# Optimization experiments

Hardware: AMD Instinct MI355X
Metric: run time of the kernel (lower is better)

## Reference

```python
import jax, jax.numpy as jnp
import numpy as np

EPS = 1e-5

def _gcn_norm(edge_index, n):
    # Add self-loops, compute symmetric normalization deg^-1/2 * deg^-1/2 (PyG GCNConv).
    src = jnp.concatenate([edge_index[0], jnp.arange(n)])
    dst = jnp.concatenate([edge_index[1], jnp.arange(n)])
    deg = jax.ops.segment_sum(jnp.ones_like(dst, dtype=jnp.float32), dst, num_segments=n)
    dinv = jnp.where(deg > 0, jax.lax.rsqrt(deg), 0.0)
    norm = dinv[src] * dinv[dst]  # [E + N]
    return src, dst, norm

def _gcn_conv(x, W, b, src, dst, norm, n):
    h = x @ W                      # linear first (out_dim < in_dim here)
    msg = h[src] * norm[:, None]   # gather + per-edge scale
    out = jax.ops.segment_sum(msg, dst, num_segments=n)  # scatter-add aggregation
    return out + b

def _bn(x, g, b):
    # BatchNorm over nodes (training-mode batch statistics, biased variance)
    mu = x.mean(axis=0)
    var = jnp.mean((x - mu) ** 2, axis=0)
    return (x - mu) * jax.lax.rsqrt(var + EPS) * g + b


def setup_inputs() -> dict:
    key = jax.random.key(0)
    N, E, F_in = 10000, 320000, 256
    ks = jax.random.split(key, 8)
    dims = [F_in, 220, 150, 100, 60, 17]
    inp = {
        'x': jax.random.normal(ks[0], (N, F_in), dtype=jnp.float32),
        'edge_index': jax.random.randint(ks[1], (2, E), 0, N, dtype=jnp.int64),
    }
    for i in range(5):
        fan_in, fan_out = dims[i], dims[i + 1]
        scale = 1.0 / np.sqrt(fan_in)
        inp[f'W{i+1}'] = jax.random.normal(ks[2 + i], (fan_in, fan_out), dtype=jnp.float32) * scale
        inp[f'b{i+1}'] = jnp.zeros((fan_out,), dtype=jnp.float32)
    for i, d in enumerate([220, 150, 100, 60]):
        inp[f'g{i+1}'] = jnp.ones((d,), dtype=jnp.float32)
        inp[f'be{i+1}'] = jnp.zeros((d,), dtype=jnp.float32)
    return inp


def reference(x, edge_index, W1, b1, W2, b2, W3, b3, W4, b4, W5, b5,
              g1, be1, g2, be2, g3, be3, g4, be4):
    n = x.shape[0]
    src, dst, norm = _gcn_norm(edge_index, n)
    h = _gcn_conv(x, W1, b1, src, dst, norm, n)
    h = _bn(jax.nn.relu(h), g1, be1)
    # dropout omitted (eval-mode identity)
    h = _gcn_conv(h, W2, b2, src, dst, norm, n)
    h = _bn(jax.nn.relu(h), g2, be2)
    h = _gcn_conv(h, W3, b3, src, dst, norm, n)
    h = _bn(jax.nn.relu(h), g3, be3)
    h = _gcn_conv(h, W4, b4, src, dst, norm, n)
    h = _bn(jax.nn.relu(h), g4, be4)
    h = _gcn_conv(h, W5, b5, src, dst, norm, n)
    return jax.nn.log_softmax(h, axis=1)
```

## Files before the change

kernel.cpp:

```cpp
#include <hip/hip_runtime.h>
#include <math.h>

typedef unsigned short ushort_t;
typedef unsigned int uint_t;
typedef unsigned long long ull_t;

__device__ __forceinline__ float bf2f(ushort_t u) {
    union { uint_t i; float f; } x; x.i = ((uint_t)u) << 16; return x.f;
}
__device__ __forceinline__ ushort_t f2bf(float f) {
    union { float f; uint_t i; } x; x.f = f;
    uint_t r = x.i + 0x7FFFu + ((x.i >> 16) & 1u);
    return (ushort_t)(r >> 16);
}

__global__ __launch_bounds__(256) void k_init(
    int* __restrict__ cnt, float* __restrict__ stats, float* __restrict__ wbias, int N)
{
    const int gt = blockIdx.x * 256 + threadIdx.x;
    const int gth = gridDim.x * 256;
    for (int i = gt; i < N; i += gth) cnt[i] = 0;
    for (int i = gt; i < 2048; i += gth) stats[i] = 0.f;
    if (gt < 256) wbias[gt] = 0.f;
}

__global__ __launch_bounds__(256) void k_hist_prep0(
    const int* __restrict__ dst, int* __restrict__ cnt, int E, int eBlk,
    const float* __restrict__ W0, ushort_t* __restrict__ Wt)
{
    if ((int)blockIdx.x < eBlk) {
        int e = blockIdx.x * 256 + threadIdx.x;
        if (e < E) atomicAdd(&cnt[dst[e]], 1);
    } else {
        int base = ((int)blockIdx.x - eBlk) * 256 + (int)threadIdx.x;
        for (int idx = base; idx < 224 * 256; idx += 56 * 256) {
            int j = idx >> 8;
            int k = idx & 255;
            float v = (j < 220) ? W0[(long)k * 220 + j] : 0.f;
            Wt[idx] = f2bf(v);
        }
    }
}

__global__ __launch_bounds__(1024) void k_scan(
    const int* __restrict__ cnt, int* __restrict__ row_start,
    int* __restrict__ cursor, float* __restrict__ dinv, int N)
{
    __shared__ int sh[1024];
    const int tid = threadIdx.x;
    const int chunk = (N + 1023) >> 10;
    int loc[16];
    const int base = tid * chunk;
    int sum = 0;
    for (int c = 0; c < chunk; ++c) {
        int i = base + c;
        int v = (i < N) ? cnt[i] : 0;
        loc[c] = sum;
        sum += v;
    }
    sh[tid] = sum;
    __syncthreads();
    for (int off = 1; off < 1024; off <<= 1) {
        int v = (tid >= off) ? sh[tid - off] : 0;
        __syncthreads();
        sh[tid] += v;
        __syncthreads();
    }
    const int excl = sh[tid] - sum;
    for (int c = 0; c < chunk; ++c) {
        int i = base + c;
        if (i < N) {
            int rs = excl + loc[c];
            row_start[i] = rs;
            cursor[i] = rs;
            dinv[i] = rsqrtf(1.0f + (float)cnt[i]);
        }
    }
    if (tid == 1023) row_start[N] = sh[1023];
}

__global__ void k_prep(const float* __restrict__ W,
                       const float* __restrict__ g, const float* __restrict__ be,
                       const float* __restrict__ cs, const float* __restrict__ cq,
                       ushort_t* __restrict__ Wt, float* __restrict__ wbias,
                       int K, int M, int Kp, int Mp, int yW, float invN)
{
    __shared__ float sm[256];
    if ((int)blockIdx.y < yW) {
        if (threadIdx.y == 0) {
            int kk = blockIdx.x * 64 + threadIdx.x;
            float sc = 0.f;
            if (kk < K) {
                float mu = cs[kk] * invN;
                float var = cq[kk] * invN - mu * mu;
                sc = g[kk] * rsqrtf(var + 1e-5f);
            }
            sm[threadIdx.x] = sc;
        }
        __syncthreads();
        int k = blockIdx.x * 64 + threadIdx.x;
        int j = blockIdx.y * 4 + threadIdx.y;
        if (k >= Kp || j >= Mp) return;
        float v = 0.f;
        if (k < K && j < M) v = sm[threadIdx.x] * W[(long)k * M + j];
        Wt[(long)j * Kp + k] = f2bf(v);
    } else {
        __shared__ float red[4][64];
        int t = threadIdx.y * 64 + threadIdx.x;
        for (int kk = t; kk < K; kk += 256) {
            float mu = cs[kk] * invN;
            float var = cq[kk] * invN - mu * mu;
            float sc = g[kk] * rsqrtf(var + 1e-5f);
            sm[kk] = be[kk] - mu * sc;
        }
        __syncthreads();
        int jl = t & 63, kg = t >> 6;
        int j = blockIdx.x * 64 + jl;
        float s = 0.f;
        if (j < M) {
            for (int k = kg; k < K; k += 4) s += sm[k] * W[(long)k * M + j];
        }
        red[kg][jl] = s;
        __syncthreads();
        if (kg == 0 && j < Mp) wbias[j] = red[0][jl] + red[1][jl] + red[2][jl] + red[3][jl];
    }
}

template<int KP, bool F32A, bool FILL>
__global__ __launch_bounds__(256) void k_gemm_mfma(
    const void* __restrict__ Xin, const ushort_t* __restrict__ Wt,
    const float* __restrict__ wbias, const float* __restrict__ dinv,
    ushort_t* __restrict__ h2, int N, int Mp,
    int gx, const int* __restrict__ fsrc, const int* __restrict__ fdst,
    int* __restrict__ fcursor, int* __restrict__ fcsr, int fE)
{
    typedef __attribute__((ext_vector_type(8))) short short8;
    typedef __attribute__((ext_vector_type(4))) float floatx4;
    constexpr int LSTR = KP + 16;
    __shared__ ushort_t Bs[64 * LSTR];

    if (FILL) {
        if ((int)blockIdx.x >= gx) {
            const int fid = ((int)blockIdx.x - gx) * (int)gridDim.y + (int)blockIdx.y;
            const int e = fid * 256 + (int)threadIdx.x;
            if (e < fE) {
                int pos = atomicAdd(&fcursor[fdst[e]], 1);
                fcsr[pos] = fsrc[e];
            }
            return;
        }
    }

    const int tid = threadIdx.x;
    const int wave = tid >> 6, lane = tid & 63;
    const int m = lane & 15, quad = lane >> 4;
    const int i0 = blockIdx.x * 64 + wave * 16;
    const int j0 = blockIdx.y * 64;
    const int ncols = min(64, Mp - j0);
    const int ntiles = ncols >> 4;

    {
        const int cpr = KP / 8;
        const int chunks = ncols * cpr;
        for (int c = tid; c < chunks; c += 256) {
            int jj = c / cpr;
            int kk = (c - jj * cpr) * 8;
            *(short8*)(Bs + jj * LSTR + kk) =
                *(const short8*)(Wt + (long)(j0 + jj) * KP + kk);
        }
    }
    __syncthreads();

    if (i0 >= N) return;

    floatx4 acc[4];
    #pragma unroll
    for (int t = 0; t < 4; ++t) { acc[t].x = 0.f; acc[t].y = 0.f; acc[t].z = 0.f; acc[t].w = 0.f; }

    const int ra = min(i0 + m, N - 1);
    const ushort_t* arow_h = F32A ? nullptr : (const ushort_t*)Xin + (long)ra * KP + quad * 8;
    const float*    arow_f = F32A ? (const float*)Xin + (long)ra * KP + quad * 8 : nullptr;

    #pragma unroll
    for (int k0 = 0; k0 < KP; k0 += 32) {
        short8 av;
        if (F32A) {
            float4 f0 = *(const float4*)(arow_f + k0);
            float4 f1 = *(const float4*)(arow_f + k0 + 4);
            av[0] = (short)f2bf(f0.x); av[1] = (short)f2bf(f0.y);
            av[2] = (short)f2bf(f0.z); av[3] = (short)f2bf(f0.w);
            av[4] = (short)f2bf(f1.x); av[5] = (short)f2bf(f1.y);
            av[6] = (short)f2bf(f1.z); av[7] = (short)f2bf(f1.w);
        } else {
            av = *(const short8*)(arow_h + k0);
        }
        #pragma unroll
        for (int t = 0; t < 4; ++t) {
            if (t < ntiles) {
                short8 bv = *(const short8*)(Bs + (t * 16 + m) * LSTR + k0 + quad * 8);
                acc[t] = __builtin_amdgcn_mfma_f32_16x16x32_bf16(av, bv, acc[t], 0, 0, 0);
            }
        }
    }

    #pragma unroll
    for (int t = 0; t < 4; ++t) {
        if (t < ntiles) {
            int j = j0 + t * 16 + m;
            float wb = wbias[j];
            #pragma unroll
            for (int r = 0; r < 4; ++r) {
                int i = i0 + quad * 4 + r;
                if (i < N) h2[(long)i * Mp + j] = f2bf((acc[t][r] + wb) * dinv[i]);
            }
        }
    }
}

__global__ __launch_bounds__(256) void k_agg(
    const int* __restrict__ row_start, const int* __restrict__ csr_src,
    const ushort_t* __restrict__ h2, int hs,
    const float* __restrict__ dinv, const float* __restrict__ b,
    ushort_t* __restrict__ tmpb, int ts,
    float* __restrict__ cs, float* __restrict__ csq,
    int N, int M, int Q, ull_t magic, uint_t sh)
{
    __shared__ float s_s[256];
    __shared__ float s_q[256];
    const int tid = threadIdx.x;
    s_s[tid] = 0.f;
    s_q[tid] = 0.f;
    __syncthreads();

    const uint_t g = blockIdx.x * 256 + tid;
    const uint_t i = (uint_t)(((ull_t)g * magic) >> sh);
    const int jp = (int)(g - i * Q);
    const int j0 = jp * 8;
    float vals[8];
    bool active = false;

    if (i < (uint_t)N) {
        if (j0 >= M) {
            *(uint4*)(tmpb + (long)i * ts + j0) = make_uint4(0u, 0u, 0u, 0u);
        } else {
            active = true;
            const int s0 = row_start[i];
            const int s1 = row_start[i + 1];
            const ushort_t* hp = h2 + j0;
            float acc[8];
            {
                uint4 v = *(const uint4*)(hp + (long)i * hs);
                acc[0] = bf2f((ushort_t)(v.x & 0xffff)); acc[1] = bf2f((ushort_t)(v.x >> 16));
                acc[2] = bf2f((ushort_t)(v.y & 0xffff)); acc[3] = bf2f((ushort_t)(v.y >> 16));
                acc[4] = bf2f((ushort_t)(v.z & 0xffff)); acc[5] = bf2f((ushort_t)(v.z >> 16));
                acc[6] = bf2f((ushort_t)(v.w & 0xffff)); acc[7] = bf2f((ushort_t)(v.w >> 16));
            }
            int e = s0;
            for (; e + 3 < s1; e += 4) {
                int n0 = csr_src[e], n1 = csr_src[e + 1], n2 = csr_src[e + 2], n3 = csr_src[e + 3];
                uint4 w0 = *(const uint4*)(hp + (long)n0 * hs);
                uint4 w1 = *(const uint4*)(hp + (long)n1 * hs);
                uint4 w2 = *(const uint4*)(hp + (long)n2 * hs);
                uint4 w3 = *(const uint4*)(hp + (long)n3 * hs);
                acc[0] += bf2f((ushort_t)(w0.x & 0xffff)); acc[1] += bf2f((ushort_t)(w0.x >> 16));
                acc[2] += bf2f((ushort_t)(w0.y & 0xffff)); acc[3] += bf2f((ushort_t)(w0.y >> 16));
                acc[4] += bf2f((ushort_t)(w0.z & 0xffff)); acc[5] += bf2f((ushort_t)(w0.z >> 16));
                acc[6] += bf2f((ushort_t)(w0.w & 0xffff)); acc[7] += bf2f((ushort_t)(w0.w >> 16));
                acc[0] += bf2f((ushort_t)(w1.x & 0xffff)); acc[1] += bf2f((ushort_t)(w1.x >> 16));
                acc[2] += bf2f((ushort_t)(w1.y & 0xffff)); acc[3] += bf2f((ushort_t)(w1.y >> 16));
                acc[4] += bf2f((ushort_t)(w1.z & 0xffff)); acc[5] += bf2f((ushort_t)(w1.z >> 16));
                acc[6] += bf2f((ushort_t)(w1.w & 0xffff)); acc[7] += bf2f((ushort_t)(w1.w >> 16));
                acc[0] += bf2f((ushort_t)(w2.x & 0xffff)); acc[1] += bf2f((ushort_t)(w2.x >> 16));
                acc[2] += bf2f((ushort_t)(w2.y & 0xffff)); acc[3] += bf2f((ushort_t)(w2.y >> 16));
                acc[4] += bf2f((ushort_t)(w2.z & 0xffff)); acc[5] += bf2f((ushort_t)(w2.z >> 16));
                acc[6] += bf2f((ushort_t)(w2.w & 0xffff)); acc[7] += bf2f((ushort_t)(w2.w >> 16));
                acc[0] += bf2f((ushort_t)(w3.x & 0xffff)); acc[1] += bf2f((ushort_t)(w3.x >> 16));
                acc[2] += bf2f((ushort_t)(w3.y & 0xffff)); acc[3] += bf2f((ushort_t)(w3.y >> 16));
                acc[4] += bf2f((ushort_t)(w3.z & 0xffff)); acc[5] += bf2f((ushort_t)(w3.z >> 16));
                acc[6] += bf2f((ushort_t)(w3.w & 0xffff)); acc[7] += bf2f((ushort_t)(w3.w >> 16));
            }
            for (; e < s1; ++e) {
                uint4 w = *(const uint4*)(hp + (long)csr_src[e] * hs);
                acc[0] += bf2f((ushort_t)(w.x & 0xffff)); acc[1] += bf2f((ushort_t)(w.x >> 16));
                acc[2] += bf2f((ushort_t)(w.y & 0xffff)); acc[3] += bf2f((ushort_t)(w.y >> 16));
                acc[4] += bf2f((ushort_t)(w.z & 0xffff)); acc[5] += bf2f((ushort_t)(w.z >> 16));
                acc[6] += bf2f((ushort_t)(w.w & 0xffff)); acc[7] += bf2f((ushort_t)(w.w >> 16));
            }
            const float di = dinv[i];
            ushort_t r[8];
            #pragma unroll
            for (int u = 0; u < 8; ++u) {
                float v = (j0 + u < M) ? fmaxf(acc[u] * di + b[j0 + u], 0.f) : 0.f;
                vals[u] = v;
                r[u] = f2bf(v);
            }
            uint4 pk;
            pk.x = (uint_t)r[0] | ((uint_t)r[1] << 16);
            pk.y = (uint_t)r[2] | ((uint_t)r[3] << 16);
            pk.z = (uint_t)r[4] | ((uint_t)r[5] << 16);
            pk.w = (uint_t)r[6] | ((uint_t)r[7] << 16);
            *(uint4*)(tmpb + (long)i * ts + j0) = pk;
        }
    }

    if (active) {
        #pragma unroll
        for (int u = 0; u < 8; ++u) {
            atomicAdd(&s_s[j0 + u], vals[u]);
            atomicAdd(&s_q[j0 + u], vals[u] * vals[u]);
        }
    }
    __syncthreads();
    if (tid < ts && (s_s[tid] != 0.f || s_q[tid] != 0.f)) {
        unsafeAtomicAdd(&cs[tid], s_s[tid]);
        unsafeAtomicAdd(&csq[tid], s_q[tid]);
    }
}

__global__ __launch_bounds__(256) void k_agg_final(
    const int* __restrict__ row_start, const int* __restrict__ csr_src,
    const ushort_t* __restrict__ h2, const float* __restrict__ dinv,
    const float* __restrict__ b, float* __restrict__ out, int N, int M)
{
    const int x = threadIdx.x;
    const int i = blockIdx.x * 16 + threadIdx.y;
    if (i >= N) return;
    const int j0 = 2 * x, j1 = 2 * x + 1;
    uint_t v = *(const uint_t*)(h2 + (long)i * 32 + j0);
    float a0 = bf2f((ushort_t)(v & 0xffff));
    float a1 = bf2f((ushort_t)(v >> 16));
    const int s0 = row_start[i];
    const int s1 = row_start[i + 1];
    int e = s0;
    for (; e + 1 < s1; e += 2) {
        int n0 = csr_src[e], n1 = csr_src[e + 1];
        uint_t w0 = *(const uint_t*)(h2 + (long)n0 * 32 + j0);
        uint_t w1 = *(const uint_t*)(h2 + (long)n1 * 32 + j0);
        a0 += bf2f((ushort_t)(w0 & 0xffff)); a1 += bf2f((ushort_t)(w0 >> 16));
        a0 += bf2f((ushort_t)(w1 & 0xffff)); a1 += bf2f((ushort_t)(w1 >> 16));
    }
    for (; e < s1; ++e) {
        uint_t w = *(const uint_t*)(h2 + (long)csr_src[e] * 32 + j0);
        a0 += bf2f((ushort_t)(w & 0xffff)); a1 += bf2f((ushort_t)(w >> 16));
    }
    const float di = dinv[i];
    float r0 = (j0 < M) ? (a0 * di + b[j0]) : -INFINITY;
    float r1 = (j1 < M) ? (a1 * di + b[j1]) : -INFINITY;
    float m = fmaxf(r0, r1);
    #pragma unroll
    for (int msk = 1; msk < 16; msk <<= 1) m = fmaxf(m, __shfl_xor(m, msk, 16));
    float s = ((j0 < M) ? expf(r0 - m) : 0.f) + ((j1 < M) ? expf(r1 - m) : 0.f);
    #pragma unroll
    for (int msk = 1; msk < 16; msk <<= 1) s += __shfl_xor(s, msk, 16);
    const float l = logf(s) + m;
    if (j0 < M) out[(long)i * M + j0] = r0 - l;
    if (j1 < M) out[(long)i * M + j1] = r1 - l;
}


static inline int pad16(int v) { return (v + 15) & ~15; }
static inline int pad32(int v) { return (v + 31) & ~31; }

extern "C" void kernel_launch(void* const* d_in, const int* in_sizes, int n_in,
                              void* d_out, int out_size, void* d_ws, size_t ws_size,
                              hipStream_t stream)
{
    const int dims[6] = {256, 220, 150, 100, 60, 17};
    const int N = in_sizes[0] / dims[0];
    const int E = in_sizes[1] / 2;

    const float* x  = (const float*)d_in[0];
    const int* ei   = (const int*)d_in[1];
    const int* srcv = ei;
    const int* dstv = ei + E;
    const float* Wl[5], *bl[5];
    for (int l = 0; l < 5; ++l) {
        Wl[l] = (const float*)d_in[2 + 2 * l];
        bl[l] = (const float*)d_in[3 + 2 * l];
    }
    const float* gl[4], *bel[4];
    for (int l = 0; l < 4; ++l) {
        gl[l]  = (const float*)d_in[12 + 2 * l];
        bel[l] = (const float*)d_in[13 + 2 * l];
    }
    float* out = (float*)d_out;

    char* w = (char*)d_ws;
    const long NB  = ((long)N * 4 + 255) & ~255L;
    const long NB1 = ((long)(N + 1) * 4 + 255) & ~255L;
    const long EB  = ((long)E * 4 + 255) & ~255L;
    const long FBB = ((long)N * 224 * 2 + 255) & ~255L;
    const long WTB = ((long)224 * 256 * 2 + 255) & ~255L;

    long o = 0;
    float* dinv      = (float*)(w + o);  o += NB;
    float* stats     = (float*)(w + o);  o += 2048 * 4;
    float* wbias     = (float*)(w + o);  o += 1024;
    int*   cnt       = (int*)(w + o);    o += NB;
    int*   row_start = (int*)(w + o);    o += NB1;
    int*   cursor    = (int*)(w + o);    o += NB;
    int*   csr_src   = (int*)(w + o);    o += EB;
    ushort_t* Wt     = (ushort_t*)(w + o); o += WTB;
    ushort_t* h2     = (ushort_t*)(w + o); o += FBB;
    ushort_t* tmpb   = (ushort_t*)(w + o); o += FBB;

    const int eBlk = (E + 255) / 256;
    const float invN = 1.0f / (float)N;

    k_init<<<(N + 255) / 256, 256, 0, stream>>>(cnt, stats, wbias, N);
    k_hist_prep0<<<eBlk + 56, 256, 0, stream>>>(dstv, cnt, E, eBlk, Wl[0], Wt);
    k_scan<<<1, 1024, 0, stream>>>(cnt, row_start, cursor, dinv, N);

    for (int l = 0; l < 5; ++l) {
        const int K  = dims[l];
        const int M  = dims[l + 1];
        const int Kp = pad32(K);
        const int Mp = pad16(M);
        const int ts = (l < 4) ? pad32(M) : 32;

        if (l > 0) {
            const int yW = (Mp + 3) / 4;
            k_prep<<<dim3((Kp + 63) / 64, yW + 1), dim3(64, 4), 0, stream>>>(
                Wl[l], gl[l - 1], bel[l - 1],
                stats + (l - 1) * 512, stats + (l - 1) * 512 + 256,
                Wt, wbias, K, M, Kp, Mp, yW, invN);
        }

        dim3 gg((N + 63) / 64, (Mp + 63) / 64);
        if (l == 0) {
            const int fx = (eBlk + (int)gg.y - 1) / (int)gg.y;
            dim3 gg0(gg.x + fx, gg.y);
            k_gemm_mfma<256, true, true><<<gg0, 256, 0, stream>>>(
                x, Wt, wbias, dinv, h2, N, Mp,
                (int)gg.x, srcv, dstv, cursor, csr_src, E);
        } else {
            switch (Kp) {
                case 224: k_gemm_mfma<224, false, false><<<gg, 256, 0, stream>>>(
                    tmpb, Wt, wbias, dinv, h2, N, Mp, 0, nullptr, nullptr, nullptr, nullptr, 0); break;
                case 160: k_gemm_mfma<160, false, false><<<gg, 256, 0, stream>>>(
                    tmpb, Wt, wbias, dinv, h2, N, Mp, 0, nullptr, nullptr, nullptr, nullptr, 0); break;
                case 128: k_gemm_mfma<128, false, false><<<gg, 256, 0, stream>>>(
                    tmpb, Wt, wbias, dinv, h2, N, Mp, 0, nullptr, nullptr, nullptr, nullptr, 0); break;
                case  64: k_gemm_mfma< 64, false, false><<<gg, 256, 0, stream>>>(
                    tmpb, Wt, wbias, dinv, h2, N, Mp, 0, nullptr, nullptr, nullptr, nullptr, 0); break;
            }
        }

        if (l < 4) {
            const int Q = ts / 8;
            uint_t shmt = 0;
            while ((1u << shmt) < (uint_t)Q) ++shmt;
            shmt += 32;
            const ull_t magic = ((1ULL << shmt) + Q - 1) / (ull_t)Q;
            const long total = (long)N * Q;
            k_agg<<<(int)((total + 255) / 256), 256, 0, stream>>>(
                row_start, csr_src, h2, Mp, dinv, bl[l], tmpb, ts,
                stats + l * 512, stats + l * 512 + 256,
                N, M, Q, magic, shmt);
        } else {
            k_agg_final<<<(N + 15) / 16, dim3(16, 16), 0, stream>>>(
                row_start, csr_src, h2, dinv, bl[l], out, N, M);
        }
    }
}
```

Measured before the change: 384.3 us.

## Split neighbor aggregation across four lanes per output chunk with shuffle reduction

```diff
diff --git a/kernel.cpp b/kernel.cpp
--- a/kernel.cpp
+++ b/kernel.cpp
@@ -223,7 +223,7 @@
     const float* __restrict__ dinv, const float* __restrict__ b,
     ushort_t* __restrict__ tmpb, int ts,
     float* __restrict__ cs, float* __restrict__ csq,
-    int N, int M, int Q, ull_t magic, uint_t sh)
+    int N, int M, int P, ull_t magic, uint_t sh)
 {
     __shared__ float s_s[256];
     __shared__ float s_q[256];
@@ -234,30 +234,35 @@
 
     const uint_t g = blockIdx.x * 256 + tid;
     const uint_t i = (uint_t)(((ull_t)g * magic) >> sh);
-    const int jp = (int)(g - i * Q);
+    const int r = (int)(g - i * (uint_t)P);
+    const int jp = r >> 2;
+    const int half = r & 3;
     const int j0 = jp * 8;
     float vals[8];
     bool active = false;
 
     if (i < (uint_t)N) {
         if (j0 >= M) {
-            *(uint4*)(tmpb + (long)i * ts + j0) = make_uint4(0u, 0u, 0u, 0u);
+            if (half == 0)
+                *(uint4*)(tmpb + (long)i * ts + j0) = make_uint4(0u, 0u, 0u, 0u);
         } else {
-            active = true;
             const int s0 = row_start[i];
             const int s1 = row_start[i + 1];
             const ushort_t* hp = h2 + j0;
             float acc[8];
-            {
+            if (half == 0) {
                 uint4 v = *(const uint4*)(hp + (long)i * hs);
                 acc[0] = bf2f((ushort_t)(v.x & 0xffff)); acc[1] = bf2f((ushort_t)(v.x >> 16));
                 acc[2] = bf2f((ushort_t)(v.y & 0xffff)); acc[3] = bf2f((ushort_t)(v.y >> 16));
                 acc[4] = bf2f((ushort_t)(v.z & 0xffff)); acc[5] = bf2f((ushort_t)(v.z >> 16));
                 acc[6] = bf2f((ushort_t)(v.w & 0xffff)); acc[7] = bf2f((ushort_t)(v.w >> 16));
-            }
-            int e = s0;
-            for (; e + 3 < s1; e += 4) {
-                int n0 = csr_src[e], n1 = csr_src[e + 1], n2 = csr_src[e + 2], n3 = csr_src[e + 3];
+            } else {
+                #pragma unroll
+                for (int u = 0; u < 8; ++u) acc[u] = 0.f;
+            }
+            int e = s0 + half;
+            for (; e + 12 < s1; e += 16) {
+                int n0 = csr_src[e], n1 = csr_src[e + 4], n2 = csr_src[e + 8], n3 = csr_src[e + 12];
                 uint4 w0 = *(const uint4*)(hp + (long)n0 * hs);
                 uint4 w1 = *(const uint4*)(hp + (long)n1 * hs);
                 uint4 w2 = *(const uint4*)(hp + (long)n2 * hs);
@@ -279,27 +284,35 @@
                 acc[4] += bf2f((ushort_t)(w3.z & 0xffff)); acc[5] += bf2f((ushort_t)(w3.z >> 16));
                 acc[6] += bf2f((ushort_t)(w3.w & 0xffff)); acc[7] += bf2f((ushort_t)(w3.w >> 16));
             }
-            for (; e < s1; ++e) {
+            for (; e < s1; e += 4) {
                 uint4 w = *(const uint4*)(hp + (long)csr_src[e] * hs);
                 acc[0] += bf2f((ushort_t)(w.x & 0xffff)); acc[1] += bf2f((ushort_t)(w.x >> 16));
                 acc[2] += bf2f((ushort_t)(w.y & 0xffff)); acc[3] += bf2f((ushort_t)(w.y >> 16));
                 acc[4] += bf2f((ushort_t)(w.z & 0xffff)); acc[5] += bf2f((ushort_t)(w.z >> 16));
                 acc[6] += bf2f((ushort_t)(w.w & 0xffff)); acc[7] += bf2f((ushort_t)(w.w >> 16));
             }
-            const float di = dinv[i];
-            ushort_t r[8];
             #pragma unroll
-            for (int u = 0; u < 8; ++u) {
-                float v = (j0 + u < M) ? fmaxf(acc[u] * di + b[j0 + u], 0.f) : 0.f;
-                vals[u] = v;
-                r[u] = f2bf(v);
-            }
-            uint4 pk;
-            pk.x = (uint_t)r[0] | ((uint_t)r[1] << 16);
-            pk.y = (uint_t)r[2] | ((uint_t)r[3] << 16);
-            pk.z = (uint_t)r[4] | ((uint_t)r[5] << 16);
-            pk.w = (uint_t)r[6] | ((uint_t)r[7] << 16);
-            *(uint4*)(tmpb + (long)i * ts + j0) = pk;
+            for (int u = 0; u < 8; ++u) acc[u] += __shfl_xor(acc[u], 1, 64);
+            #pragma unroll
+            for (int u = 0; u < 8; ++u) acc[u] += __shfl_xor(acc[u], 2, 64);
+
+            if (half == 0) {
+                const float di = dinv[i];
+                ushort_t rr[8];
+                #pragma unroll
+                for (int u = 0; u < 8; ++u) {
+                    float v = (j0 + u < M) ? fmaxf(acc[u] * di + b[j0 + u], 0.f) : 0.f;
+                    vals[u] = v;
+                    rr[u] = f2bf(v);
+                }
+                uint4 pk;
+                pk.x = (uint_t)rr[0] | ((uint_t)rr[1] << 16);
+                pk.y = (uint_t)rr[2] | ((uint_t)rr[3] << 16);
+                pk.z = (uint_t)rr[4] | ((uint_t)rr[5] << 16);
+                pk.w = (uint_t)rr[6] | ((uint_t)rr[7] << 16);
+                *(uint4*)(tmpb + (long)i * ts + j0) = pk;
+                active = true;
+            }
         }
     }
 
@@ -322,27 +335,37 @@
     const ushort_t* __restrict__ h2, const float* __restrict__ dinv,
     const float* __restrict__ b, float* __restrict__ out, int N, int M)
 {
-    const int x = threadIdx.x;
-    const int i = blockIdx.x * 16 + threadIdx.y;
+    const int tid = threadIdx.x;
+    const int lane = tid & 63;
+    const int wv = tid >> 6;
+    const int i = blockIdx.x * 4 + wv;
+    const int x = lane & 15;
+    const int half = lane >> 4;
     if (i >= N) return;
     const int j0 = 2 * x, j1 = 2 * x + 1;
-    uint_t v = *(const uint_t*)(h2 + (long)i * 32 + j0);
-    float a0 = bf2f((ushort_t)(v & 0xffff));
-    float a1 = bf2f((ushort_t)(v >> 16));
+    float a0 = 0.f, a1 = 0.f;
+    if (half == 0) {
+        uint_t v = *(const uint_t*)(h2 + (long)i * 32 + j0);
+        a0 = bf2f((ushort_t)(v & 0xffff));
+        a1 = bf2f((ushort_t)(v >> 16));
+    }
     const int s0 = row_start[i];
     const int s1 = row_start[i + 1];
-    int e = s0;
-    for (; e + 1 < s1; e += 2) {
-        int n0 = csr_src[e], n1 = csr_src[e + 1];
+    int e = s0 + half;
+    for (; e + 4 < s1; e += 8) {
+        int n0 = csr_src[e], n1 = csr_src[e + 4];
         uint_t w0 = *(const uint_t*)(h2 + (long)n0 * 32 + j0);
         uint_t w1 = *(const uint_t*)(h2 + (long)n1 * 32 + j0);
         a0 += bf2f((ushort_t)(w0 & 0xffff)); a1 += bf2f((ushort_t)(w0 >> 16));
         a0 += bf2f((ushort_t)(w1 & 0xffff)); a1 += bf2f((ushort_t)(w1 >> 16));
     }
-    for (; e < s1; ++e) {
+    for (; e < s1; e += 4) {
         uint_t w = *(const uint_t*)(h2 + (long)csr_src[e] * 32 + j0);
         a0 += bf2f((ushort_t)(w & 0xffff)); a1 += bf2f((ushort_t)(w >> 16));
     }
+    a0 += __shfl_xor(a0, 16, 64); a0 += __shfl_xor(a0, 32, 64);
+    a1 += __shfl_xor(a1, 16, 64); a1 += __shfl_xor(a1, 32, 64);
+
     const float di = dinv[i];
     float r0 = (j0 < M) ? (a0 * di + b[j0]) : -INFINITY;
     float r1 = (j1 < M) ? (a1 * di + b[j1]) : -INFINITY;
@@ -353,8 +376,10 @@
     #pragma unroll
     for (int msk = 1; msk < 16; msk <<= 1) s += __shfl_xor(s, msk, 16);
     const float l = logf(s) + m;
-    if (j0 < M) out[(long)i * M + j0] = r0 - l;
-    if (j1 < M) out[(long)i * M + j1] = r1 - l;
+    if (half == 0) {
+        if (j0 < M) out[(long)i * M + j0] = r0 - l;
+        if (j1 < M) out[(long)i * M + j1] = r1 - l;
+    }
 }
 
 
@@ -448,17 +473,18 @@
 
         if (l < 4) {
             const int Q = ts / 8;
+            const int P = 4 * Q;
             uint_t shmt = 0;
-            while ((1u << shmt) < (uint_t)Q) ++shmt;
+            while ((1u << shmt) < (uint_t)P) ++shmt;
             shmt += 32;
-            const ull_t magic = ((1ULL << shmt) + Q - 1) / (ull_t)Q;
-            const long total = (long)N * Q;
+            const ull_t magic = ((1ULL << shmt) + P - 1) / (ull_t)P;
+            const long total = (long)N * P;
             k_agg<<<(int)((total + 255) / 256), 256, 0, stream>>>(
                 row_start, csr_src, h2, Mp, dinv, bl[l], tmpb, ts,
                 stats + l * 512, stats + l * 512 + 256,
-                N, M, Q, magic, shmt);
+                N, M, P, magic, shmt);
         } else {
-            k_agg_final<<<(N + 15) / 16, dim3(16, 16), 0, stream>>>(
+            k_agg_final<<<(N + 3) / 4, 256, 0, stream>>>(
                 row_start, csr_src, h2, dinv, bl[l], out, N, M);
         }
     }
```

New measurement: 561.9 us. 46.2% more time.
